# Kernel optimization log

Measured on AMD Instinct MI355X. Metric: run time of the kernel, lower is better.

## Reference

```python
import jax, jax.numpy as jnp
import numpy as np

B, S, D = 8, 2048, 512

def setup_inputs() -> dict:
    key = jax.random.key(0)
    ks = jax.random.split(key, 9)
    scale = 1.0 / np.sqrt(D)
    q = jax.random.normal(ks[0], (B, S, D), dtype=jnp.float32)
    k = jax.random.normal(ks[1], (B, S, D), dtype=jnp.float32)
    v = jax.random.normal(ks[2], (B, S, D), dtype=jnp.float32)
    # causal mask, broadcast over batch: True = attend
    mask = jnp.tril(jnp.ones((S, S), dtype=bool))[None, :, :]
    Wq = jax.random.normal(ks[3], (D, D), dtype=jnp.float32) * scale
    bq = jax.random.normal(ks[4], (D,), dtype=jnp.float32) * scale
    Wk = jax.random.normal(ks[5], (D, D), dtype=jnp.float32) * scale
    bk = jax.random.normal(ks[6], (D,), dtype=jnp.float32) * scale
    Wv = jax.random.normal(ks[7], (D, D), dtype=jnp.float32) * scale
    bv = jax.random.normal(ks[8], (D,), dtype=jnp.float32) * scale
    return {"q": q, "k": k, "v": v, "mask": mask,
            "Wq": Wq, "bq": bq, "Wk": Wk, "bk": bk, "Wv": Wv, "bv": bv}

def reference(q, k, v, mask, Wq, bq, Wk, bk, Wv, bv):
    # torch nn.Linear: x @ W^T + b
    Q = jnp.einsum('bsd,ed->bse', q, Wq) + bq
    K = jnp.einsum('bsd,ed->bse', k, Wk) + bk
    V = jnp.einsum('bsd,ed->bse', v, Wv) + bv
    scores = jnp.einsum('bqd,bkd->bqk', Q, K) / jnp.sqrt(jnp.float32(D))
    scores = jnp.where(mask, scores, jnp.float32(-1e9))
    prob = jax.nn.softmax(scores, axis=-1)
    out = jnp.einsum('bqk,bkd->bqd', prob, V)
    return out
```

## Files before the change

### kernel.cpp

```cpp
#include <hip/hip_runtime.h>
#include <stdint.h>
#include <stddef.h>
#include <math.h>

typedef _Float16 half8 __attribute__((ext_vector_type(8)));
typedef float f32x4 __attribute__((ext_vector_type(4)));

#define SCALE_QK 0.04419417382415922f

__device__ __forceinline__ void gload16(const void* g, void* lds) {
  __builtin_amdgcn_global_load_lds(
      (const __attribute__((address_space(1))) void*)g,
      (__attribute__((address_space(3))) void*)lds,
      16, 0, 0);
}

template<bool A_F32>
__device__ __forceinline__ void run_kloop(const void* Arow0, const _Float16* Brow0,
                                          int lda, int ldb, int kIters,
                                          _Float16* As, _Float16 (*Bs)[128*64],
                                          f32x4 (&acc)[4][4])
{
  const int tid  = threadIdx.x;
  const int lane = tid & 63;
  const int w    = tid >> 6;
  const int wm   = w >> 1, wn = w & 1;
  const int srow = tid >> 3;
  const int sg   = tid & 7;
  const int swz  = sg ^ (srow & 7);
  const int fr   = lane & 15;
  const int fq   = lane >> 4;
  const int fx   = lane & 7;

  f32x4 preF[8];
  half8 preH[4];

  auto loadA = [&](int it) {
    const int k0 = it * 64;
    if constexpr (A_F32) {
      const float* A = (const float*)Arow0;
      #pragma unroll
      for (int i = 0; i < 4; ++i) {
        const float* src = A + (size_t)(i*32 + srow) * lda + (k0 + sg*8);
        preF[2*i]   = *(const f32x4*)src;
        preF[2*i+1] = *(const f32x4*)(src + 4);
      }
    } else {
      const _Float16* A = (const _Float16*)Arow0;
      #pragma unroll
      for (int i = 0; i < 4; ++i)
        preH[i] = *(const half8*)(A + (size_t)(i*32 + srow) * lda + (k0 + sg*8));
    }
  };
  auto writeA = [&]() {
    #pragma unroll
    for (int i = 0; i < 4; ++i) {
      half8 h;
      if constexpr (A_F32) {
        f32x4 x = preF[2*i], y = preF[2*i+1];
        h[0]=(_Float16)x[0]; h[1]=(_Float16)x[1]; h[2]=(_Float16)x[2]; h[3]=(_Float16)x[3];
        h[4]=(_Float16)y[0]; h[5]=(_Float16)y[1]; h[6]=(_Float16)y[2]; h[7]=(_Float16)y[3];
      } else {
        h = preH[i];
      }
      *(half8*)(As + (i*32 + srow)*64 + swz*8) = h;
    }
  };
  auto gloadB = [&](int it, _Float16* dstBs) {
    const int k0 = it * 64;
    #pragma unroll
    for (int i = 0; i < 4; ++i)
      gload16(Brow0 + (size_t)(i*32 + srow) * ldb + (k0 + swz*8), dstBs + i*2048 + w*512);
  };
  auto compute = [&](const _Float16* cBs) {
    #pragma unroll
    for (int ks = 0; ks < 2; ++ks) {
      half8 av[4], bv[4];
      const int slot = (ks*4 + fq) ^ fx;
      #pragma unroll
      for (int i = 0; i < 4; ++i) {
        av[i] = *(const half8*)(As + (wm*64 + i*16 + fr)*64 + slot*8);
        bv[i] = *(const half8*)(cBs + (wn*64 + i*16 + fr)*64 + slot*8);
      }
      #pragma unroll
      for (int i = 0; i < 4; ++i) {
        #pragma unroll
        for (int j = 0; j < 4; ++j)
          acc[i][j] = __builtin_amdgcn_mfma_f32_16x16x32_f16(av[i], bv[j], acc[i][j], 0, 0, 0);
      }
    }
  };

  loadA(0);
  gloadB(0, Bs[0]);
  writeA();
  __syncthreads();

  for (int it = 0; it < kIters; ++it) {
    const int cur = it & 1;
    const bool more = (it + 1) < kIters;
    if (more) {
      gloadB(it + 1, Bs[cur ^ 1]);
      loadA(it + 1);
    }
    compute(Bs[cur]);
    __syncthreads();
    if (more) writeA();
    __syncthreads();
  }
}

__global__ __launch_bounds__(256) void k_cvtw(const float* __restrict__ Wq,
                                              const float* __restrict__ Wk,
                                              const float* __restrict__ Wv,
                                              _Float16* __restrict__ Wb)
{
  const int t = blockIdx.x * 256 + threadIdx.x;
  const int base = t * 8;
  const int z = base >> 18;
  const int off = base & 262143;
  const float* src = (z == 0) ? Wq : ((z == 1) ? Wk : Wv);
  f32x4 a = *(const f32x4*)(src + off);
  f32x4 b = *(const f32x4*)(src + off + 4);
  half8 h;
  h[0]=(_Float16)a[0]; h[1]=(_Float16)a[1]; h[2]=(_Float16)a[2]; h[3]=(_Float16)a[3];
  h[4]=(_Float16)b[0]; h[5]=(_Float16)b[1]; h[6]=(_Float16)b[2]; h[7]=(_Float16)b[3];
  *(half8*)(Wb + base) = h;
}

__global__ __launch_bounds__(256) void k_proj(const float* __restrict__ q,
                                              const float* __restrict__ k,
                                              const float* __restrict__ v,
                                              const _Float16* __restrict__ Wb,
                                              const float* __restrict__ bq,
                                              const float* __restrict__ bk,
                                              const float* __restrict__ bv,
                                              _Float16* __restrict__ Qb,
                                              _Float16* __restrict__ Kb,
                                              _Float16* __restrict__ Vb)
{
  __shared__ __align__(16) _Float16 As[128*64];
  __shared__ __align__(16) _Float16 Bs[2][128*64];
  const int bid = blockIdx.x;
  const int xcd = bid & 7, i = bid >> 3;
  const int p = xcd * 48 + (i >> 2);
  const int nt = i & 3;
  const int z = p >> 7, mt = p & 127;

  const float* A     = (z == 0) ? q  : (z == 1) ? k  : v;
  const float* bia   = (z == 0) ? bq : (z == 1) ? bk : bv;
  const _Float16* B  = Wb + (size_t)z * 512 * 512;
  _Float16* C        = (z == 0) ? Qb : (z == 1) ? Kb : Vb;

  f32x4 acc[4][4] = {};
  run_kloop<true>(A + (size_t)mt*128*512, B + (size_t)nt*128*512, 512, 512, 8, As, Bs, acc);

  const int lane = threadIdx.x & 63, w = threadIdx.x >> 6;
  const int wm = w >> 1, wn = w & 1;
  const int fr = lane & 15, fq = lane >> 4;
  #pragma unroll
  for (int j = 0; j < 4; ++j) {
    const int col = nt*128 + wn*64 + j*16 + fr;
    const float bval = bia[col];
    #pragma unroll
    for (int i2 = 0; i2 < 4; ++i2) {
      const int row = mt*128 + wm*64 + i2*16 + fq*4;
      #pragma unroll
      for (int r = 0; r < 4; ++r)
        C[(size_t)(row + r) * 512 + col] = (_Float16)(acc[i2][j][r] + bval);
    }
  }
}

__global__ __launch_bounds__(256) void k_trans(const _Float16* __restrict__ Vb,
                                               _Float16* __restrict__ Vt)
{
  __shared__ __align__(16) _Float16 t[64][72];
  const int st = blockIdx.x, dt = blockIdx.y, b = blockIdx.z;
  const int r = threadIdx.x >> 2, g = threadIdx.x & 3;
  const _Float16* src = Vb + ((size_t)b*2048 + st*64 + r)*512 + dt*64 + g*16;
  half8 v0 = *(const half8*)src;
  half8 v1 = *(const half8*)(src + 8);
  *(half8*)&t[r][g*16]     = v0;
  *(half8*)&t[r][g*16 + 8] = v1;
  __syncthreads();
  half8 o0, o1;
  #pragma unroll
  for (int i2 = 0; i2 < 8; ++i2) o0[i2] = t[g*16 + i2][r];
  #pragma unroll
  for (int i2 = 0; i2 < 8; ++i2) o1[i2] = t[g*16 + 8 + i2][r];
  _Float16* dst = Vt + ((size_t)b*512 + dt*64 + r)*2048 + st*64 + g*16;
  *(half8*)dst       = o0;
  *(half8*)(dst + 8) = o1;
}

__global__ __launch_bounds__(256) void k_scores(const _Float16* __restrict__ Qb,
                                                const _Float16* __restrict__ Kb,
                                                _Float16* __restrict__ P)
{
  const int bid = blockIdx.x;
  const int b = bid & 7;
  const int t = bid >> 3;
  int qt = (int)((sqrtf(8.0f * (float)t + 1.0f) - 1.0f) * 0.5f);
  int base = (qt * (qt + 1)) >> 1;
  if (t < base)                { --qt; base = (qt * (qt + 1)) >> 1; }
  else if (t >= base + qt + 1) { ++qt; base = (qt * (qt + 1)) >> 1; }
  const int kt = t - base;

  __shared__ __align__(16) _Float16 As[128*64];
  __shared__ __align__(16) _Float16 Bs[2][128*64];
  f32x4 acc[4][4] = {};
  run_kloop<false>(Qb + ((size_t)b*2048 + qt*128)*512,
                   Kb + ((size_t)b*2048 + kt*128)*512,
                   512, 512, 8, As, Bs, acc);
  const int lane = threadIdx.x & 63, w = threadIdx.x >> 6;
  const int wm = w >> 1, wn = w & 1;
  const int fr = lane & 15, fq = lane >> 4;
  #pragma unroll
  for (int i = 0; i < 4; ++i) {
    const int row = qt*128 + wm*64 + i*16 + fq*4;
    #pragma unroll
    for (int j = 0; j < 4; ++j) {
      const int col = kt*128 + wn*64 + j*16 + fr;
      #pragma unroll
      for (int r = 0; r < 4; ++r)
        P[((size_t)b*2048 + row + r) * 2048 + col] = (_Float16)(acc[i][j][r] * SCALE_QK);
    }
  }
}

__global__ __launch_bounds__(256) void k_softmax(_Float16* __restrict__ P)
{
  const int lane = threadIdx.x & 63;
  const int row  = blockIdx.x * 4 + (threadIdx.x >> 6);
  const int qIdx = row & 2047;
  _Float16* p = P + (size_t)row * 2048;
  const int L    = qIdx + 1;
  const int Lpad = ((qIdx >> 7) + 1) * 128;

  float m = -1e30f, s = 0.f;
  for (int i0 = lane * 8; i0 < L; i0 += 512) {
    float xv[8];
    if (i0 + 8 <= L) {
      half8 x = *(const half8*)(p + i0);
      #pragma unroll
      for (int j = 0; j < 8; ++j) xv[j] = (float)x[j];
    } else {
      #pragma unroll
      for (int j = 0; j < 8; ++j) xv[j] = (i0 + j < L) ? (float)p[i0 + j] : -1e30f;
    }
    float cm = xv[0];
    #pragma unroll
    for (int j = 1; j < 8; ++j) cm = fmaxf(cm, xv[j]);
    const float mn = fmaxf(m, cm);
    float cs = 0.f;
    #pragma unroll
    for (int j = 0; j < 8; ++j) cs += __expf(xv[j] - mn);
    s = s * __expf(m - mn) + cs;
    m = mn;
  }
  #pragma unroll
  for (int d = 1; d < 64; d <<= 1) {
    const float mo = __shfl_xor(m, d, 64);
    const float so = __shfl_xor(s, d, 64);
    const float mn = fmaxf(m, mo);
    s = s * __expf(m - mn) + so * __expf(mo - mn);
    m = mn;
  }
  const float inv = 1.0f / s;

  for (int i0 = lane * 8; i0 < Lpad; i0 += 512) {
    half8 o;
    if (i0 + 8 <= L) {
      half8 x = *(const half8*)(p + i0);
      #pragma unroll
      for (int j = 0; j < 8; ++j) o[j] = (_Float16)(__expf((float)x[j] - m) * inv);
    } else {
      #pragma unroll
      for (int j = 0; j < 8; ++j) {
        const int idx = i0 + j;
        o[j] = (idx < L) ? (_Float16)(__expf((float)p[idx] - m) * inv) : (_Float16)0.f;
      }
    }
    *(half8*)(p + i0) = o;
  }
}

__global__ __launch_bounds__(256) void k_pv(const _Float16* __restrict__ P,
                                            const _Float16* __restrict__ Vt,
                                            float* __restrict__ Out)
{
  const int bid = blockIdx.x;
  const int b = bid & 7;
  const int r0 = bid >> 3;
  const int qi = r0 >> 2, dt = r0 & 3;
  const int qt = (qi & 1) ? (15 - (qi >> 1)) : (qi >> 1);

  __shared__ __align__(16) _Float16 As[128*64];
  __shared__ __align__(16) _Float16 Bs[2][128*64];
  f32x4 acc[4][4] = {};
  run_kloop<false>(P  + ((size_t)b*2048 + qt*128)*2048,
                   Vt + ((size_t)b*512  + dt*128)*2048,
                   2048, 2048, (qt + 1) * 2, As, Bs, acc);
  const int lane = threadIdx.x & 63, w = threadIdx.x >> 6;
  const int wm = w >> 1, wn = w & 1;
  const int fr = lane & 15, fq = lane >> 4;
  #pragma unroll
  for (int i = 0; i < 4; ++i) {
    const int row = qt*128 + wm*64 + i*16 + fq*4;
    #pragma unroll
    for (int j = 0; j < 4; ++j) {
      const int col = dt*128 + wn*64 + j*16 + fr;
      #pragma unroll
      for (int r = 0; r < 4; ++r)
        Out[((size_t)b*2048 + row + r) * 512 + col] = acc[i][j][r];
    }
  }
}

extern "C" void kernel_launch(void* const* d_in, const int* in_sizes, int n_in,
                              void* d_out, int out_size, void* d_ws, size_t ws_size,
                              hipStream_t stream) {
  (void)in_sizes; (void)n_in; (void)out_size;
  const float* q  = (const float*)d_in[0];
  const float* k  = (const float*)d_in[1];
  const float* v  = (const float*)d_in[2];
  const float* Wq = (const float*)d_in[4];
  const float* bq = (const float*)d_in[5];
  const float* Wk = (const float*)d_in[6];
  const float* bk = (const float*)d_in[7];
  const float* Wv = (const float*)d_in[8];
  const float* bv = (const float*)d_in[9];

  const size_t OFF_P  = 0;
  const size_t OFF_Q  = (size_t)64 << 20;
  const size_t OFF_K  = (size_t)80 << 20;
  const size_t OFF_V  = (size_t)96 << 20;
  const size_t OFF_VT = (size_t)112 << 20;
  const size_t OFF_W  = (size_t)128 << 20;
  const size_t NEEDED = OFF_W + (size_t)3 * 512 * 512 * sizeof(_Float16);
  if (ws_size < NEEDED) return;

  char* ws = (char*)d_ws;
  _Float16* P  = (_Float16*)(ws + OFF_P);
  _Float16* Qb = (_Float16*)(ws + OFF_Q);
  _Float16* Kb = (_Float16*)(ws + OFF_K);
  _Float16* Vb = (_Float16*)(ws + OFF_V);
  _Float16* Vt = (_Float16*)(ws + OFF_VT);
  _Float16* Wb = (_Float16*)(ws + OFF_W);
  float* Out = (float*)d_out;

  k_cvtw   <<<dim3(384),      dim3(256), 0, stream>>>(Wq, Wk, Wv, Wb);
  k_proj   <<<dim3(1536),     dim3(256), 0, stream>>>(q, k, v, Wb, bq, bk, bv, Qb, Kb, Vb);
  k_trans  <<<dim3(32, 8, 8), dim3(256), 0, stream>>>(Vb, Vt);
  k_scores <<<dim3(1088),     dim3(256), 0, stream>>>(Qb, Kb, P);
  k_softmax<<<dim3(4096),     dim3(256), 0, stream>>>(P);
  k_pv     <<<dim3(512),      dim3(256), 0, stream>>>(P, Vt, Out);
}
```

Before: 282.8 us.

## Pre-convert inputs to fp16 and load both GEMM operands via direct-to-LDS loads

Adds a separate kernel that converts q/k/v to fp16 into the P workspace region. The shared GEMM k-loop then loads both A and B tiles with global_load_lds instead of going through registers for A. LDS double buffering of B is dropped: a single buffer with barriers around each stage, which cuts LDS usage and may raise occupancy. The cost is an extra conversion pass over 48MB of inputs and no overlap of global loads with MFMA compute inside a block.

Result: no change. 283.2 us (+0.2%).

```diff
diff --git a/kernel.cpp b/kernel.cpp
--- a/kernel.cpp
+++ b/kernel.cpp
@@ -15,10 +15,9 @@
       16, 0, 0);
 }
 
-template<bool A_F32>
-__device__ __forceinline__ void run_kloop(const void* Arow0, const _Float16* Brow0,
+__device__ __forceinline__ void run_kloop(const _Float16* A, const _Float16* B,
                                           int lda, int ldb, int kIters,
-                                          _Float16* As, _Float16 (*Bs)[128*64],
+                                          _Float16* As, _Float16* Bs,
                                           f32x4 (&acc)[4][4])
 {
   const int tid  = threadIdx.x;
@@ -32,47 +31,15 @@
   const int fq   = lane >> 4;
   const int fx   = lane & 7;
 
-  f32x4 preF[8];
-  half8 preH[4];
-
-  auto loadA = [&](int it) {
+  auto stage = [&](int it) {
     const int k0 = it * 64;
-    if constexpr (A_F32) {
-      const float* A = (const float*)Arow0;
-      #pragma unroll
-      for (int i = 0; i < 4; ++i) {
-        const float* src = A + (size_t)(i*32 + srow) * lda + (k0 + sg*8);
-        preF[2*i]   = *(const f32x4*)src;
-        preF[2*i+1] = *(const f32x4*)(src + 4);
-      }
-    } else {
-      const _Float16* A = (const _Float16*)Arow0;
-      #pragma unroll
-      for (int i = 0; i < 4; ++i)
-        preH[i] = *(const half8*)(A + (size_t)(i*32 + srow) * lda + (k0 + sg*8));
+    #pragma unroll
+    for (int i = 0; i < 4; ++i) {
+      gload16(A + (size_t)(i*32 + srow) * lda + (k0 + swz*8), As + i*2048 + w*512);
+      gload16(B + (size_t)(i*32 + srow) * ldb + (k0 + swz*8), Bs + i*2048 + w*512);
     }
   };
-  auto writeA = [&]() {
-    #pragma unroll
-    for (int i = 0; i < 4; ++i) {
-      half8 h;
-      if constexpr (A_F32) {
-        f32x4 x = preF[2*i], y = preF[2*i+1];
-        h[0]=(_Float16)x[0]; h[1]=(_Float16)x[1]; h[2]=(_Float16)x[2]; h[3]=(_Float16)x[3];
-        h[4]=(_Float16)y[0]; h[5]=(_Float16)y[1]; h[6]=(_Float16)y[2]; h[7]=(_Float16)y[3];
-      } else {
-        h = preH[i];
-      }
-      *(half8*)(As + (i*32 + srow)*64 + swz*8) = h;
-    }
-  };
-  auto gloadB = [&](int it, _Float16* dstBs) {
-    const int k0 = it * 64;
-    #pragma unroll
-    for (int i = 0; i < 4; ++i)
-      gload16(Brow0 + (size_t)(i*32 + srow) * ldb + (k0 + swz*8), dstBs + i*2048 + w*512);
-  };
-  auto compute = [&](const _Float16* cBs) {
+  auto compute = [&]() {
     #pragma unroll
     for (int ks = 0; ks < 2; ++ks) {
       half8 av[4], bv[4];
@@ -80,7 +47,7 @@
       #pragma unroll
       for (int i = 0; i < 4; ++i) {
         av[i] = *(const half8*)(As + (wm*64 + i*16 + fr)*64 + slot*8);
-        bv[i] = *(const half8*)(cBs + (wn*64 + i*16 + fr)*64 + slot*8);
+        bv[i] = *(const half8*)(Bs + (wn*64 + i*16 + fr)*64 + slot*8);
       }
       #pragma unroll
       for (int i = 0; i < 4; ++i) {
@@ -91,21 +58,13 @@
     }
   };
 
-  loadA(0);
-  gloadB(0, Bs[0]);
-  writeA();
+  stage(0);
   __syncthreads();
-
-  for (int it = 0; it < kIters; ++it) {
-    const int cur = it & 1;
-    const bool more = (it + 1) < kIters;
-    if (more) {
-      gloadB(it + 1, Bs[cur ^ 1]);
-      loadA(it + 1);
-    }
-    compute(Bs[cur]);
+  for (int it = 0; ; ) {
+    compute();
+    if (++it >= kIters) break;
     __syncthreads();
-    if (more) writeA();
+    stage(it);
     __syncthreads();
   }
 }
@@ -128,9 +87,25 @@
   *(half8*)(Wb + base) = h;
 }
 
-__global__ __launch_bounds__(256) void k_proj(const float* __restrict__ q,
-                                              const float* __restrict__ k,
-                                              const float* __restrict__ v,
+__global__ __launch_bounds__(256) void k_cvtin(const float* __restrict__ q,
+                                               const float* __restrict__ k,
+                                               const float* __restrict__ v,
+                                               _Float16* __restrict__ X)
+{
+  const size_t t = (size_t)blockIdx.x * 256 + threadIdx.x;
+  const size_t base = t * 8;
+  const int z = (int)(base >> 23);
+  const size_t off = base & 8388607;
+  const float* src = (z == 0) ? q : ((z == 1) ? k : v);
+  f32x4 a = *(const f32x4*)(src + off);
+  f32x4 b = *(const f32x4*)(src + off + 4);
+  half8 h;
+  h[0]=(_Float16)a[0]; h[1]=(_Float16)a[1]; h[2]=(_Float16)a[2]; h[3]=(_Float16)a[3];
+  h[4]=(_Float16)b[0]; h[5]=(_Float16)b[1]; h[6]=(_Float16)b[2]; h[7]=(_Float16)b[3];
+  *(half8*)(X + base) = h;
+}
+
+__global__ __launch_bounds__(256) void k_proj(const _Float16* __restrict__ X,
                                               const _Float16* __restrict__ Wb,
                                               const float* __restrict__ bq,
                                               const float* __restrict__ bk,
@@ -140,20 +115,20 @@
                                               _Float16* __restrict__ Vb)
 {
   __shared__ __align__(16) _Float16 As[128*64];
-  __shared__ __align__(16) _Float16 Bs[2][128*64];
+  __shared__ __align__(16) _Float16 Bs[128*64];
   const int bid = blockIdx.x;
   const int xcd = bid & 7, i = bid >> 3;
   const int p = xcd * 48 + (i >> 2);
   const int nt = i & 3;
   const int z = p >> 7, mt = p & 127;
 
-  const float* A     = (z == 0) ? q  : (z == 1) ? k  : v;
+  const _Float16* A  = X + (size_t)z * 8388608;
   const float* bia   = (z == 0) ? bq : (z == 1) ? bk : bv;
   const _Float16* B  = Wb + (size_t)z * 512 * 512;
   _Float16* C        = (z == 0) ? Qb : (z == 1) ? Kb : Vb;
 
   f32x4 acc[4][4] = {};
-  run_kloop<true>(A + (size_t)mt*128*512, B + (size_t)nt*128*512, 512, 512, 8, As, Bs, acc);
+  run_kloop(A + (size_t)mt*128*512, B + (size_t)nt*128*512, 512, 512, 8, As, Bs, acc);
 
   const int lane = threadIdx.x & 63, w = threadIdx.x >> 6;
   const int wm = w >> 1, wn = w & 1;
@@ -208,11 +183,11 @@
   const int kt = t - base;
 
   __shared__ __align__(16) _Float16 As[128*64];
-  __shared__ __align__(16) _Float16 Bs[2][128*64];
+  __shared__ __align__(16) _Float16 Bs[128*64];
   f32x4 acc[4][4] = {};
-  run_kloop<false>(Qb + ((size_t)b*2048 + qt*128)*512,
-                   Kb + ((size_t)b*2048 + kt*128)*512,
-                   512, 512, 8, As, Bs, acc);
+  run_kloop(Qb + ((size_t)b*2048 + qt*128)*512,
+            Kb + ((size_t)b*2048 + kt*128)*512,
+            512, 512, 8, As, Bs, acc);
   const int lane = threadIdx.x & 63, w = threadIdx.x >> 6;
   const int wm = w >> 1, wn = w & 1;
   const int fr = lane & 15, fq = lane >> 4;
@@ -297,11 +272,11 @@
   const int qt = (qi & 1) ? (15 - (qi >> 1)) : (qi >> 1);
 
   __shared__ __align__(16) _Float16 As[128*64];
-  __shared__ __align__(16) _Float16 Bs[2][128*64];
+  __shared__ __align__(16) _Float16 Bs[128*64];
   f32x4 acc[4][4] = {};
-  run_kloop<false>(P  + ((size_t)b*2048 + qt*128)*2048,
-                   Vt + ((size_t)b*512  + dt*128)*2048,
-                   2048, 2048, (qt + 1) * 2, As, Bs, acc);
+  run_kloop(P  + ((size_t)b*2048 + qt*128)*2048,
+            Vt + ((size_t)b*512  + dt*128)*2048,
+            2048, 2048, (qt + 1) * 2, As, Bs, acc);
   const int lane = threadIdx.x & 63, w = threadIdx.x >> 6;
   const int wm = w >> 1, wn = w & 1;
   const int fr = lane & 15, fq = lane >> 4;
@@ -343,6 +318,7 @@
 
   char* ws = (char*)d_ws;
   _Float16* P  = (_Float16*)(ws + OFF_P);
+  _Float16* X  = (_Float16*)(ws + OFF_P);
   _Float16* Qb = (_Float16*)(ws + OFF_Q);
   _Float16* Kb = (_Float16*)(ws + OFF_K);
   _Float16* Vb = (_Float16*)(ws + OFF_V);
@@ -351,7 +327,8 @@
   float* Out = (float*)d_out;
 
   k_cvtw   <<<dim3(384),      dim3(256), 0, stream>>>(Wq, Wk, Wv, Wb);
-  k_proj   <<<dim3(1536),     dim3(256), 0, stream>>>(q, k, v, Wb, bq, bk, bv, Qb, Kb, Vb);
+  k_cvtin  <<<dim3(12288),    dim3(256), 0, stream>>>(q, k, v, X);
+  k_proj   <<<dim3(1536),     dim3(256), 0, stream>>>(X, Wb, bq, bk, bv, Qb, Kb, Vb);
   k_trans  <<<dim3(32, 8, 8), dim3(256), 0, stream>>>(Vb, Vt);
   k_scores <<<dim3(1088),     dim3(256), 0, stream>>>(Qb, Kb, P);
   k_softmax<<<dim3(4096),     dim3(256), 0, stream>>>(P);
```
